# Kernel tuning notes

Hardware: AMD Instinct MI355X
Metric: run time of the kernel (lower is better)

## Reference

```python
import jax, jax.numpy as jnp
import numpy as np

B, C, H, W = 2, 72, 96, 96
FACTOR = 4  # input_dim // output_dim = 72 // 18


def setup_inputs() -> dict:
    key = jax.random.key(0)
    ks = jax.random.split(key, 7)
    s = 1.0 / np.sqrt(C)
    return {
        "x": jax.random.normal(ks[0], (B, C, H, W), dtype=jnp.float32),
        "Wq": jax.random.normal(ks[1], (C, C), dtype=jnp.float32) * s,
        "bq": jax.random.normal(ks[2], (C,), dtype=jnp.float32) * 0.01,
        "Wk": jax.random.normal(ks[3], (C, C), dtype=jnp.float32) * s,
        "bk": jax.random.normal(ks[4], (C,), dtype=jnp.float32) * 0.01,
        "Wv": jax.random.normal(ks[5], (C, C), dtype=jnp.float32) * s,
        "bv": jax.random.normal(ks[6], (C,), dtype=jnp.float32) * 0.01,
    }


def reference(x, Wq, bq, Wk, bk, Wv, bv):
    b, c, h, w = x.shape
    n = h * w
    flat = x.reshape(b, c, n)  # [B, C, N]
    # 1x1 convs == per-pixel channel matmuls
    q = jnp.einsum('dc,bcn->bdn', Wq, flat) + bq[None, :, None]
    k = jnp.einsum('dc,bcn->bdn', Wk, flat) + bk[None, :, None]
    v = jnp.einsum('dc,bcn->bdn', Wv, flat) + bv[None, :, None]
    # scores[b,i,j] = sum_c q[b,c,i] * k[b,c,j]  (no 1/sqrt(d) scaling, as in source)
    scores = jnp.einsum('bci,bcj->bij', q, k)  # [B, N, N]
    attn = jax.nn.softmax(scores, axis=-1)
    # weighted_values = bmm(v, attn^T): wv[b,c,i] = sum_j v[b,c,j] * attn[b,i,j]
    wv = jnp.einsum('bcj,bij->bci', v, attn)  # [B, C, N]
    wv = wv.reshape(b, c // FACTOR, FACTOR, h, w)
    xg = x.reshape(b, c // FACTOR, FACTOR, h, w)
    pooled = jnp.sum(xg * wv, axis=2)  # [B, C//FACTOR, H, W]
    return pooled
```

## Files before the change

kernel.cpp:

```cpp
#include <hip/hip_runtime.h>

#define NPIX 9216
#define CIN 72
#define CP 96
#define SPLITS 8
#define JCHUNK (NPIX / SPLITS)
#define JTILES (JCHUNK / 64)
#define L2E   1.44269504088896f
#define EXPB  46.1662413084468f

typedef __attribute__((ext_vector_type(8))) short bf16x8;
typedef __attribute__((ext_vector_type(8))) _Float16 f16x8;
typedef __attribute__((ext_vector_type(4))) float f32x4;

#define MFMA_BF16(A,B,C) __builtin_amdgcn_mfma_f32_16x16x32_bf16(A,B,C,0,0,0)
#define MFMA_F16(A,B,C)  __builtin_amdgcn_mfma_f32_16x16x32_f16(A,B,C,0,0,0)

static __device__ __forceinline__ unsigned short f2bf(float f) {
  unsigned u = __float_as_uint(f);
  u += 0x7fffu + ((u >> 16) & 1u);
  return (unsigned short)(u >> 16);
}
static __device__ __forceinline__ float bf2f(unsigned short h) {
  return __uint_as_float(((unsigned)h) << 16);
}
static __device__ __forceinline__ unsigned short f2h(float f) {
  _Float16 h = (_Float16)f;
  return *(unsigned short*)&h;
}
static __device__ __forceinline__ unsigned pack_bf_trunc(float lo, float hi) {
  return (__float_as_uint(lo) >> 16) | (__float_as_uint(hi) & 0xffff0000u);
}

__global__ __launch_bounds__(256) void wprep_kernel(
    const float* __restrict__ Wq, const float* __restrict__ Wk,
    const float* __restrict__ Wv,
    unsigned short* __restrict__ WH, unsigned short* __restrict__ WL)
{
  int id = blockIdx.x * 256 + threadIdx.x;
  if (id >= 3 * 80 * 96) return;
  int mat = id / (80 * 96);
  int rem = id % (80 * 96);
  int d = rem / 96, c = rem % 96;
  const float* W = (mat == 0) ? Wq : (mat == 1) ? Wk : Wv;
  float v = (d < 72 && c < 72) ? W[d * 72 + c] : 0.f;
  unsigned short hi = f2bf(v);
  WH[id] = hi;
  WL[id] = f2bf(v - bf2f(hi));
}

#define XTS 104

__global__ __launch_bounds__(64) void qkv_kernel(
    const float* __restrict__ x,
    const unsigned short* __restrict__ WH, const unsigned short* __restrict__ WL,
    const float* __restrict__ bq, const float* __restrict__ bk,
    const float* __restrict__ bv,
    unsigned short* __restrict__ QH, unsigned short* __restrict__ KH,
    unsigned short* __restrict__ VG)
{
  __shared__ __align__(16) unsigned short xth[16 * XTS];
  __shared__ __align__(16) unsigned short xtl[16 * XTS];
  __shared__ __align__(16) unsigned short obuf[16 * XTS];

  const int t    = threadIdx.x;
  const int quad = t >> 4;
  const int l15  = t & 15;
  const int bid  = blockIdx.x;
  const int b    = bid / 576;
  const int n0   = (bid % 576) * 16;

  for (int e = t; e < 72 * 16; e += 64) {
    int c = e >> 4, px = e & 15;
    float f = x[((size_t)b * CIN + c) * NPIX + n0 + px];
    unsigned short hi = f2bf(f);
    xth[px * XTS + c] = hi;
    xtl[px * XTS + c] = f2bf(f - bf2f(hi));
  }
  for (int e = t; e < 24 * 16; e += 64) {
    int c = 72 + (e >> 4), px = e & 15;
    xth[px * XTS + c] = 0;
    xtl[px * XTS + c] = 0;
  }
  __syncthreads();

  bf16x8 xbh[3], xbl[3];
#pragma unroll
  for (int ks = 0; ks < 3; ++ks) {
    int off = l15 * XTS + ks * 32 + quad * 8;
    xbh[ks] = *(const bf16x8*)(xth + off);
    xbl[ks] = *(const bf16x8*)(xtl + off);
  }

  for (int mat = 0; mat < 3; ++mat) {
    const unsigned short* wh = WH + mat * 80 * 96;
    const unsigned short* wl = WL + mat * 80 * 96;
    const float* bias = (mat == 0) ? bq : (mat == 1) ? bk : bv;

    f32x4 acc[5];
#pragma unroll
    for (int dm = 0; dm < 5; ++dm) {
      acc[dm] = (f32x4){0.f, 0.f, 0.f, 0.f};
#pragma unroll
      for (int ks = 0; ks < 3; ++ks) {
        bf16x8 ah = *(const bf16x8*)(wh + (dm * 16 + l15) * 96 + ks * 32 + quad * 8);
        bf16x8 al = *(const bf16x8*)(wl + (dm * 16 + l15) * 96 + ks * 32 + quad * 8);
        acc[dm] = MFMA_BF16(ah, xbh[ks], acc[dm]);
        acc[dm] = MFMA_BF16(ah, xbl[ks], acc[dm]);
        acc[dm] = MFMA_BF16(al, xbh[ks], acc[dm]);
      }
    }

    if (mat < 2) {
      __syncthreads();
#pragma unroll
      for (int dm = 0; dm < 5; ++dm)
#pragma unroll
        for (int r = 0; r < 4; ++r) {
          int d = dm * 16 + quad * 4 + r;
          float v = acc[dm][r] + (d < 72 ? bias[d] : 0.f);
          obuf[l15 * XTS + d] = f2h(v);
        }
      __syncthreads();
      unsigned short* outp = (mat == 0) ? QH : KH;
      const size_t ob = ((size_t)b * NPIX + n0) * CP;
      uint4 z; z.x = z.y = z.z = z.w = 0u;
      for (int f = t; f < 192; f += 64) {
        int row = f / 12, col = f % 12;
        *(uint4*)(outp + ob + (size_t)row * CP + col * 8) =
            (col < 10) ? *(const uint4*)(obuf + row * XTS + col * 8) : z;
      }
    } else {
#pragma unroll
      for (int dm = 0; dm < 5; ++dm)
#pragma unroll
        for (int r = 0; r < 4; ++r) {
          int d = dm * 16 + quad * 4 + r;
          float v = (d < 72) ? acc[dm][r] + bias[d] : (d == 72 ? 1.0f : 0.f);
          VG[((size_t)b * 80 + d) * NPIX + n0 + l15] = f2bf(v);
        }
    }
  }
}

#define KSP 104
#define VSP 72
#define PSP 72

__global__ __launch_bounds__(256, 3) void flash_kernel(
    const unsigned short* __restrict__ QH, const unsigned short* __restrict__ KH,
    const unsigned short* __restrict__ VG,
    unsigned short* __restrict__ OPH, float* __restrict__ LPART)
{
  __shared__ __align__(16) unsigned short ls_kh[64 * KSP];
  __shared__ __align__(16) unsigned short ls_vs[80 * VSP];
  __shared__ __align__(16) unsigned short ps[4][48 * PSP];

  const int t    = threadIdx.x;
  const int w    = t >> 6;
  const int lane = t & 63;
  const int quad = lane >> 4;
  const int l15  = lane & 15;

  const int bid  = blockIdx.x;
  const int sp   = bid & 7;
  const int slot = bid >> 3;
  const int b    = slot / 48;
  const int it   = slot % 48;
  const int i0w  = it * 192 + w * 48;

  f16x8 qh[3][3];
#pragma unroll
  for (int mi = 0; mi < 3; ++mi)
#pragma unroll
    for (int ks = 0; ks < 3; ++ks) {
      size_t off = ((size_t)b * NPIX + i0w + mi * 16 + l15) * CP + ks * 32 + quad * 8;
      qh[mi][ks] = *(const f16x8*)(QH + off);
    }

  f32x4 oacc[3][5];
#pragma unroll
  for (int mi = 0; mi < 3; ++mi)
#pragma unroll
    for (int nt = 0; nt < 5; ++nt) oacc[mi][nt] = (f32x4){0.f, 0.f, 0.f, 0.f};

  unsigned short* psw = ps[w];

  const unsigned short* kpg = KH + ((size_t)b * NPIX + sp * JCHUNK) * CP;
  const unsigned short* vpg = VG + (size_t)b * 80 * NPIX + sp * JCHUNK;

  for (int jt = 0; jt < JTILES; ++jt, kpg += 64 * CP, vpg += 64) {
    for (int idx = t; idx < 768; idx += 256) {
      int r = idx / 12, c = idx % 12;
      *(uint4*)(ls_kh + r * KSP + c * 8) = *(const uint4*)(kpg + r * CP + c * 8);
    }
    for (int idx = t; idx < 640; idx += 256) {
      int r = idx >> 3, c = idx & 7;
      *(uint4*)(ls_vs + r * VSP + c * 8) =
          *(const uint4*)(vpg + (size_t)r * NPIX + c * 8);
    }
    __syncthreads();

#pragma unroll
    for (int tj = 0; tj < 4; ++tj) {
      f16x8 fkh[3];
#pragma unroll
      for (int ks = 0; ks < 3; ++ks)
        fkh[ks] = *(const f16x8*)(ls_kh + (tj * 16 + l15) * KSP + ks * 32 + quad * 8);
#pragma unroll
      for (int mi = 0; mi < 3; ++mi) {
        f32x4 s = (f32x4){0.f, 0.f, 0.f, 0.f};
        s = MFMA_F16(fkh[0], qh[mi][0], s);
        s = MFMA_F16(fkh[1], qh[mi][1], s);
        s = MFMA_F16(fkh[2], qh[mi][2], s);
        float p0 = __builtin_amdgcn_exp2f(__builtin_fmaf(s[0], L2E, -EXPB));
        float p1 = __builtin_amdgcn_exp2f(__builtin_fmaf(s[1], L2E, -EXPB));
        float p2 = __builtin_amdgcn_exp2f(__builtin_fmaf(s[2], L2E, -EXPB));
        float p3 = __builtin_amdgcn_exp2f(__builtin_fmaf(s[3], L2E, -EXPB));
        uint2 pk;
        pk.x = pack_bf_trunc(p0, p1);
        pk.y = pack_bf_trunc(p2, p3);
        *(uint2*)(psw + (mi * 16 + l15) * PSP + tj * 16 + quad * 4) = pk;
      }
    }

#pragma unroll
    for (int js = 0; js < 2; ++js) {
      bf16x8 pf[3];
#pragma unroll
      for (int mi = 0; mi < 3; ++mi)
        pf[mi] = *(const bf16x8*)(psw + (mi * 16 + l15) * PSP + js * 32 + quad * 8);
#pragma unroll
      for (int nt = 0; nt < 5; ++nt) {
        bf16x8 vf = *(const bf16x8*)(ls_vs + (nt * 16 + l15) * VSP + js * 32 + quad * 8);
#pragma unroll
        for (int mi = 0; mi < 3; ++mi)
          oacc[mi][nt] = MFMA_BF16(vf, pf[mi], oacc[mi][nt]);
      }
    }
    __syncthreads();
  }

  const size_t sb = (size_t)(sp * 2 + b);
#pragma unroll
  for (int mi = 0; mi < 3; ++mi) {
    if (quad == 2)
      LPART[sb * NPIX + i0w + mi * 16 + l15] = oacc[mi][4][0];
    const size_t nbase = sb * 72 * (size_t)NPIX + (size_t)(i0w + mi * 16 + l15);
#pragma unroll
    for (int nt = 0; nt < 5; ++nt)
#pragma unroll
      for (int r = 0; r < 4; ++r) {
        int c = nt * 16 + quad * 4 + r;
        if (c < 72)
          OPH[(size_t)c * NPIX + nbase] = f2bf(oacc[mi][nt][r]);
      }
  }
}

__global__ __launch_bounds__(256) void combine_pool_kernel(
    const float* __restrict__ x, const unsigned short* __restrict__ OPH,
    const float* __restrict__ LPART, float* __restrict__ out)
{
  int id = blockIdx.x * 256 + threadIdx.x;
  if (id >= 2 * 18 * (NPIX / 2)) return;
  int n = (id % (NPIX / 2)) * 2;
  int rest = id / (NPIX / 2);
  int g = rest % 18, b = rest / 18;

  float2 L = make_float2(0.f, 0.f);
  float2 a0 = L, a1 = L, a2 = L, a3 = L;
#pragma unroll
  for (int s = 0; s < SPLITS; ++s) {
    size_t sb = (size_t)(s * 2 + b);
    float2 l2 = *(const float2*)(LPART + sb * NPIX + n);
    L.x += l2.x; L.y += l2.y;
    size_t base = (sb * 72 + g * 4) * NPIX + n;
    unsigned u0 = *(const unsigned*)(OPH + base);
    unsigned u1 = *(const unsigned*)(OPH + base + NPIX);
    unsigned u2 = *(const unsigned*)(OPH + base + 2 * NPIX);
    unsigned u3 = *(const unsigned*)(OPH + base + 3 * NPIX);
    a0.x += __uint_as_float(u0 << 16); a0.y += __uint_as_float(u0 & 0xffff0000u);
    a1.x += __uint_as_float(u1 << 16); a1.y += __uint_as_float(u1 & 0xffff0000u);
    a2.x += __uint_as_float(u2 << 16); a2.y += __uint_as_float(u2 & 0xffff0000u);
    a3.x += __uint_as_float(u3 << 16); a3.y += __uint_as_float(u3 & 0xffff0000u);
  }
  size_t xb = ((size_t)b * CIN + g * 4) * NPIX + n;
  float2 x0 = *(const float2*)(x + xb);
  float2 x1 = *(const float2*)(x + xb + NPIX);
  float2 x2 = *(const float2*)(x + xb + 2 * NPIX);
  float2 x3 = *(const float2*)(x + xb + 3 * NPIX);
  float2 r;
  r.x = (x0.x * a0.x + x1.x * a1.x + x2.x * a2.x + x3.x * a3.x) / L.x;
  r.y = (x0.y * a0.y + x1.y * a1.y + x2.y * a2.y + x3.y * a3.y) / L.y;
  *(float2*)(out + (size_t)id * 2) = r;
}

extern "C" void kernel_launch(void* const* d_in, const int* in_sizes, int n_in,
                              void* d_out, int out_size, void* d_ws, size_t ws_size,
                              hipStream_t stream) {
  const float* x  = (const float*)d_in[0];
  const float* Wq = (const float*)d_in[1];
  const float* bq = (const float*)d_in[2];
  const float* Wk = (const float*)d_in[3];
  const float* bk = (const float*)d_in[4];
  const float* Wv = (const float*)d_in[5];
  const float* bv = (const float*)d_in[6];
  float* out = (float*)d_out;

  char* p = (char*)d_ws;
  const size_t szQK = (size_t)2 * NPIX * CP * 2;
  unsigned short* QH = (unsigned short*)p; p += szQK;
  unsigned short* KH = (unsigned short*)p; p += szQK;
  unsigned short* VG = (unsigned short*)p; p += (size_t)2 * 80 * NPIX * 2;
  unsigned short* WH = (unsigned short*)p; p += (size_t)3 * 80 * 96 * 2;
  unsigned short* WL = (unsigned short*)p; p += (size_t)3 * 80 * 96 * 2;
  unsigned short* OPH = (unsigned short*)p; p += (size_t)SPLITS * 2 * 72 * NPIX * 2;
  float* LPART = (float*)p; p += (size_t)SPLITS * 2 * NPIX * 4;

  wprep_kernel<<<(3 * 80 * 96 + 255) / 256, 256, 0, stream>>>(Wq, Wk, Wv, WH, WL);
  qkv_kernel<<<1152, 64, 0, stream>>>(x, WH, WL, bq, bk, bv, QH, KH, VG);
  flash_kernel<<<768, 256, 0, stream>>>(QH, KH, VG, OPH, LPART);
  combine_pool_kernel<<<(2 * 18 * (NPIX / 2) + 255) / 256, 256, 0, stream>>>(
      x, OPH, LPART, out);
}
```

Baseline: 171.1 us.

## Fuse x-weighted pooling into flash epilogue and load K tiles via global_load_lds

The flash kernel epilogue now multiplies each partial output by x and sums groups of four channels, writing one fp32 numerator per group instead of 72 bf16 channels per split. The combine kernel then only sums numerators and denominators across splits and divides. This cuts the partial-output traffic and drops the x reads from the combine step. K tiles are also copied straight to LDS with global_load_lds, with the K row padding removed, and the qkv kernel reads x as float4. The risks are more LDS bank conflicts without padding and extra x loads inside the flash epilogue.

```diff
diff --git a/kernel.cpp b/kernel.cpp
--- a/kernel.cpp
+++ b/kernel.cpp
@@ -30,6 +30,12 @@
 }
 static __device__ __forceinline__ unsigned pack_bf_trunc(float lo, float hi) {
   return (__float_as_uint(lo) >> 16) | (__float_as_uint(hi) & 0xffff0000u);
+}
+static __device__ __forceinline__ void load_lds16(const unsigned short* g,
+                                                  unsigned short* l) {
+  __builtin_amdgcn_global_load_lds(
+      (const __attribute__((address_space(1))) unsigned int*)g,
+      (__attribute__((address_space(3))) unsigned int*)l, 16, 0, 0);
 }
 
 __global__ __launch_bounds__(256) void wprep_kernel(
@@ -70,12 +76,16 @@
   const int b    = bid / 576;
   const int n0   = (bid % 576) * 16;
 
-  for (int e = t; e < 72 * 16; e += 64) {
-    int c = e >> 4, px = e & 15;
-    float f = x[((size_t)b * CIN + c) * NPIX + n0 + px];
-    unsigned short hi = f2bf(f);
-    xth[px * XTS + c] = hi;
-    xtl[px * XTS + c] = f2bf(f - bf2f(hi));
+  for (int e = t; e < 288; e += 64) {
+    int c = e >> 2, f4 = (e & 3) * 4;
+    float4 xv = *(const float4*)(x + ((size_t)b * CIN + c) * NPIX + n0 + f4);
+    float vv[4] = {xv.x, xv.y, xv.z, xv.w};
+#pragma unroll
+    for (int k = 0; k < 4; ++k) {
+      unsigned short hi = f2bf(vv[k]);
+      xth[(f4 + k) * XTS + c] = hi;
+      xtl[(f4 + k) * XTS + c] = f2bf(vv[k] - bf2f(hi));
+    }
   }
   for (int e = t; e < 24 * 16; e += 64) {
     int c = 72 + (e >> 4), px = e & 15;
@@ -143,14 +153,15 @@
   }
 }
 
-#define KSP 104
+#define KSP 96
 #define VSP 72
 #define PSP 72
 
 __global__ __launch_bounds__(256, 3) void flash_kernel(
+    const float* __restrict__ x,
     const unsigned short* __restrict__ QH, const unsigned short* __restrict__ KH,
     const unsigned short* __restrict__ VG,
-    unsigned short* __restrict__ OPH, float* __restrict__ LPART)
+    float* __restrict__ NUM, float* __restrict__ LPART)
 {
   __shared__ __align__(16) unsigned short ls_kh[64 * KSP];
   __shared__ __align__(16) unsigned short ls_vs[80 * VSP];
@@ -190,9 +201,10 @@
   const unsigned short* vpg = VG + (size_t)b * 80 * NPIX + sp * JCHUNK;
 
   for (int jt = 0; jt < JTILES; ++jt, kpg += 64 * CP, vpg += 64) {
-    for (int idx = t; idx < 768; idx += 256) {
-      int r = idx / 12, c = idx % 12;
-      *(uint4*)(ls_kh + r * KSP + c * 8) = *(const uint4*)(kpg + r * CP + c * 8);
+#pragma unroll
+    for (int k = 0; k < 3; ++k) {
+      int chunk = w + k * 4;
+      load_lds16(kpg + chunk * 512 + lane * 8, ls_kh + chunk * 512);
     }
     for (int idx = t; idx < 640; idx += 256) {
       int r = idx >> 3, c = idx & 7;
@@ -244,56 +256,47 @@
   const size_t sb = (size_t)(sp * 2 + b);
 #pragma unroll
   for (int mi = 0; mi < 3; ++mi) {
+    const int i = i0w + mi * 16 + l15;
     if (quad == 2)
-      LPART[sb * NPIX + i0w + mi * 16 + l15] = oacc[mi][4][0];
-    const size_t nbase = sb * 72 * (size_t)NPIX + (size_t)(i0w + mi * 16 + l15);
-#pragma unroll
-    for (int nt = 0; nt < 5; ++nt)
-#pragma unroll
-      for (int r = 0; r < 4; ++r) {
-        int c = nt * 16 + quad * 4 + r;
-        if (c < 72)
-          OPH[(size_t)c * NPIX + nbase] = f2bf(oacc[mi][nt][r]);
-      }
+      LPART[sb * NPIX + i] = oacc[mi][4][0];
+#pragma unroll
+    for (int nt = 0; nt < 5; ++nt) {
+      int c0 = nt * 16 + quad * 4;
+      if (c0 < 72) {
+        float num = 0.f;
+#pragma unroll
+        for (int r = 0; r < 4; ++r)
+          num = __builtin_fmaf(x[((size_t)b * CIN + c0 + r) * NPIX + i],
+                               oacc[mi][nt][r], num);
+        NUM[(sb * 18 + (c0 >> 2)) * NPIX + i] = num;
+      }
+    }
   }
 }
 
 __global__ __launch_bounds__(256) void combine_pool_kernel(
-    const float* __restrict__ x, const unsigned short* __restrict__ OPH,
-    const float* __restrict__ LPART, float* __restrict__ out)
+    const float* __restrict__ NUM, const float* __restrict__ LPART,
+    float* __restrict__ out)
 {
   int id = blockIdx.x * 256 + threadIdx.x;
-  if (id >= 2 * 18 * (NPIX / 2)) return;
-  int n = (id % (NPIX / 2)) * 2;
-  int rest = id / (NPIX / 2);
+  if (id >= 2 * 18 * (NPIX / 4)) return;
+  int n = (id % (NPIX / 4)) * 4;
+  int rest = id / (NPIX / 4);
   int g = rest % 18, b = rest / 18;
 
-  float2 L = make_float2(0.f, 0.f);
-  float2 a0 = L, a1 = L, a2 = L, a3 = L;
+  float4 A = make_float4(0.f, 0.f, 0.f, 0.f);
+  float4 L = make_float4(0.f, 0.f, 0.f, 0.f);
 #pragma unroll
   for (int s = 0; s < SPLITS; ++s) {
     size_t sb = (size_t)(s * 2 + b);
-    float2 l2 = *(const float2*)(LPART + sb * NPIX + n);
-    L.x += l2.x; L.y += l2.y;
-    size_t base = (sb * 72 + g * 4) * NPIX + n;
-    unsigned u0 = *(const unsigned*)(OPH + base);
-    unsigned u1 = *(const unsigned*)(OPH + base + NPIX);
-    unsigned u2 = *(const unsigned*)(OPH + base + 2 * NPIX);
-    unsigned u3 = *(const unsigned*)(OPH + base + 3 * NPIX);
-    a0.x += __uint_as_float(u0 << 16); a0.y += __uint_as_float(u0 & 0xffff0000u);
-    a1.x += __uint_as_float(u1 << 16); a1.y += __uint_as_float(u1 & 0xffff0000u);
-    a2.x += __uint_as_float(u2 << 16); a2.y += __uint_as_float(u2 & 0xffff0000u);
-    a3.x += __uint_as_float(u3 << 16); a3.y += __uint_as_float(u3 & 0xffff0000u);
-  }
-  size_t xb = ((size_t)b * CIN + g * 4) * NPIX + n;
-  float2 x0 = *(const float2*)(x + xb);
-  float2 x1 = *(const float2*)(x + xb + NPIX);
-  float2 x2 = *(const float2*)(x + xb + 2 * NPIX);
-  float2 x3 = *(const float2*)(x + xb + 3 * NPIX);
-  float2 r;
-  r.x = (x0.x * a0.x + x1.x * a1.x + x2.x * a2.x + x3.x * a3.x) / L.x;
-  r.y = (x0.y * a0.y + x1.y * a1.y + x2.y * a2.y + x3.y * a3.y) / L.y;
-  *(float2*)(out + (size_t)id * 2) = r;
+    float4 a = *(const float4*)(NUM + (sb * 18 + g) * NPIX + n);
+    float4 l = *(const float4*)(LPART + sb * NPIX + n);
+    A.x += a.x; A.y += a.y; A.z += a.z; A.w += a.w;
+    L.x += l.x; L.y += l.y; L.z += l.z; L.w += l.w;
+  }
+  float4 r;
+  r.x = A.x / L.x; r.y = A.y / L.y; r.z = A.z / L.z; r.w = A.w / L.w;
+  *(float4*)(out + (size_t)id * 4) = r;
 }
 
 extern "C" void kernel_launch(void* const* d_in, const int* in_sizes, int n_in,
@@ -315,12 +318,12 @@
   unsigned short* VG = (unsigned short*)p; p += (size_t)2 * 80 * NPIX * 2;
   unsigned short* WH = (unsigned short*)p; p += (size_t)3 * 80 * 96 * 2;
   unsigned short* WL = (unsigned short*)p; p += (size_t)3 * 80 * 96 * 2;
-  unsigned short* OPH = (unsigned short*)p; p += (size_t)SPLITS * 2 * 72 * NPIX * 2;
+  float* NUM = (float*)p; p += (size_t)SPLITS * 2 * 18 * NPIX * 4;
   float* LPART = (float*)p; p += (size_t)SPLITS * 2 * NPIX * 4;
 
   wprep_kernel<<<(3 * 80 * 96 + 255) / 256, 256, 0, stream>>>(Wq, Wk, Wv, WH, WL);
   qkv_kernel<<<1152, 64, 0, stream>>>(x, WH, WL, bq, bk, bv, QH, KH, VG);
-  flash_kernel<<<768, 256, 0, stream>>>(QH, KH, VG, OPH, LPART);
-  combine_pool_kernel<<<(2 * 18 * (NPIX / 2) + 255) / 256, 256, 0, stream>>>(
-      x, OPH, LPART, out);
-}
+  flash_kernel<<<768, 256, 0, stream>>>(x, QH, KH, VG, NUM, LPART);
+  combine_pool_kernel<<<(2 * 18 * (NPIX / 4) + 255) / 256, 256, 0, stream>>>(
+      NUM, LPART, out);
+}
```

Measured after the change: 160.4 us. -6.2%, faster.
